# Optimization experiments

Measured on AMD Instinct MI355X. Metric: run time of the kernel, lower is better.

Reference implementation:

```python
import jax, jax.numpy as jnp
import numpy as np

B, N, GN, GS = 16, 100000, 4096, 64  # batch, points, num_groups, group_size


def setup_inputs() -> dict:
    key = jax.random.key(0)
    k1, k2, k3 = jax.random.split(key, 3)
    x_proto = jax.random.normal(k1, (B, N, 3), dtype=jnp.float32)
    template = jax.random.normal(k2, (N, 3), dtype=jnp.float32)
    groups = jax.random.randint(k3, (GN, GS), 0, N, dtype=jnp.int32)
    return {"x_proto": x_proto, "template": template, "groups": groups}


def reference(x_proto, template, groups):
    # x_proto: [B, N, 3], template: [N, 3], groups: [GN, GS] int indices
    b, n, _ = x_proto.shape
    Yg = template[groups]                      # [GN, GS, 3] gathered template
    Xg = x_proto[:, groups]                    # [B, GN, GS, 3] gathered current points

    # Kabsch: align template group Y to current X (R @ Y + t ~ X)
    muY = Yg.mean(axis=1)                      # [GN, 3]
    muX = Xg.mean(axis=2)                      # [B, GN, 3]
    Yc = Yg - muY[:, None, :]
    Xc = Xg - muX[:, :, None, :]
    H = jnp.einsum('gni,bgnj->bgij', Yc, Xc)   # [B, GN, 3, 3] covariance
    U, S, Vh = jnp.linalg.svd(H)
    V = jnp.swapaxes(Vh, -2, -1)
    R0 = V @ jnp.swapaxes(U, -2, -1)
    det = jnp.linalg.det(R0)                   # [B, GN]
    # flip last column of V where det < 0 to get a proper rotation
    s = jnp.where(det < 0, -1.0, 1.0).astype(x_proto.dtype)
    col_scale = jnp.stack([jnp.ones_like(s), jnp.ones_like(s), s], axis=-1)  # [B, GN, 3]
    R = (V * col_scale[..., None, :]) @ jnp.swapaxes(U, -2, -1)              # [B, GN, 3, 3]
    t = muX - jnp.einsum('bgij,gj->bgi', R, muY)                             # [B, GN, 3]

    # project template group through (R, t)
    Xg_proj = jnp.einsum('bgij,gnj->bgni', R, Yg) + t[:, :, None, :]         # [B, GN, GS, 3]

    # scatter-add with overlap counting, then average
    flat_idx = groups.reshape(-1)              # [GN*GS]
    out = jnp.zeros_like(x_proto).at[:, flat_idx].add(Xg_proj.reshape(b, -1, 3))
    counts = jnp.zeros((n,), dtype=x_proto.dtype).at[flat_idx].add(1.0)
    counts = jnp.maximum(counts, 1.0)
    return out / counts[None, :, None]
```

## Files before the change

kernel.cpp:

```cpp
#include <hip/hip_runtime.h>
#include <math.h>

static constexpr int BB = 16;
static constexpr int NN = 100000;
static constexpr int GN = 4096;
static constexpr int GS = 64;
static constexpr int NP = BB * GN;
static constexpr int NE = GN * GS;
static constexpr int NBLK = (NN + 255) / 256;

__device__ __forceinline__ float wsum64(float v) {
#pragma unroll
  for (int off = 32; off > 0; off >>= 1) v += __shfl_xor(v, off, 64);
  return v;
}

__global__ __launch_bounds__(256) void k_xpad(
    const float4* __restrict__ x, const float4* __restrict__ tpl,
    float4* __restrict__ x4, float4* __restrict__ tpl4,
    int4* __restrict__ cnt4, int* __restrict__ gtotal) {
  int t = blockIdx.x * 256 + threadIdx.x;
  if (t == 0) *gtotal = 0;
  if (t < NN / 4) {
    cnt4[t] = make_int4(0, 0, 0, 0);
    float4 a = tpl[t * 3 + 0], b = tpl[t * 3 + 1], c = tpl[t * 3 + 2];
    tpl4[t * 4 + 0] = make_float4(a.x, a.y, a.z, 0.f);
    tpl4[t * 4 + 1] = make_float4(a.w, b.x, b.y, 0.f);
    tpl4[t * 4 + 2] = make_float4(b.z, b.w, c.x, 0.f);
    tpl4[t * 4 + 3] = make_float4(c.y, c.z, c.w, 0.f);
  }
  if (t >= BB * NN / 4) return;
  float4 a = x[t * 3 + 0], b = x[t * 3 + 1], c = x[t * 3 + 2];
  x4[t * 4 + 0] = make_float4(a.x, a.y, a.z, 0.f);
  x4[t * 4 + 1] = make_float4(a.w, b.x, b.y, 0.f);
  x4[t * 4 + 2] = make_float4(b.z, b.w, c.x, 0.f);
  x4[t * 4 + 3] = make_float4(c.y, c.z, c.w, 0.f);
}

__global__ __launch_bounds__(256) void k_tpl(
    const float4* __restrict__ tpl4, const int* __restrict__ groups,
    float* __restrict__ Yg, float* __restrict__ GmY, int* __restrict__ cnt) {
  int g    = blockIdx.x * 4 + (threadIdx.x >> 6);
  int lane = threadIdx.x & 63;
  int idx = groups[g * GS + lane];
  atomicAdd(&cnt[idx], 1);
  float4 y = tpl4[idx];
  float* o = Yg + ((size_t)g * GS + lane) * 3;
  o[0] = y.x; o[1] = y.y; o[2] = y.z;
  float sy0 = wsum64(y.x), sy1 = wsum64(y.y), sy2 = wsum64(y.z);
  if (lane == 0) {
    const float inv = 1.0f / 64.0f;
    *(float4*)(GmY + (size_t)g * 4) =
        make_float4(sy0 * inv, sy1 * inv, sy2 * inv, 0.0f);
  }
}

__global__ __launch_bounds__(256) void k_stats(
    const float4* __restrict__ x4, const float* __restrict__ Yg,
    const float* __restrict__ GmY, const int* __restrict__ groups,
    float* __restrict__ Ht) {
  int bid  = (blockIdx.x & 7) * 512 + (blockIdx.x >> 3);
  int wid4 = bid * 4 + (threadIdx.x >> 6);
  int lane = threadIdx.x & 63;
  int s    = lane >> 4;
  int l4   = lane & 15;
  int p = wid4 * 4 + s;
  int b = p >> 12;
  int g = p & (GN - 1);

  int4 iv = *(const int4*)(groups + (size_t)g * GS + l4 * 4);
  const float4* yv = (const float4*)(Yg + ((size_t)g * GS + l4 * 4) * 3);
  float4 ya = yv[0], yb = yv[1], yc = yv[2];

  const float4* xb4 = x4 + (size_t)b * NN;
  float sx0 = 0.f, sx1 = 0.f, sx2 = 0.f;
  float h00 = 0.f, h01 = 0.f, h02 = 0.f;
  float h10 = 0.f, h11 = 0.f, h12 = 0.f;
  float h20 = 0.f, h21 = 0.f, h22 = 0.f;

#define ACC(Y0, Y1, Y2, IDX)                                   \
  {                                                            \
    float4 xv = xb4[IDX];                                      \
    sx0 += xv.x; sx1 += xv.y; sx2 += xv.z;                     \
    h00 += (Y0) * xv.x; h01 += (Y0) * xv.y; h02 += (Y0) * xv.z;\
    h10 += (Y1) * xv.x; h11 += (Y1) * xv.y; h12 += (Y1) * xv.z;\
    h20 += (Y2) * xv.x; h21 += (Y2) * xv.y; h22 += (Y2) * xv.z;\
  }
  ACC(ya.x, ya.y, ya.z, iv.x);
  ACC(ya.w, yb.x, yb.y, iv.y);
  ACC(yb.z, yb.w, yc.x, iv.z);
  ACC(yc.y, yc.z, yc.w, iv.w);
#undef ACC

#define RED(V)                                                 \
  V += __shfl_xor(V, 8, 64); V += __shfl_xor(V, 4, 64);        \
  V += __shfl_xor(V, 2, 64); V += __shfl_xor(V, 1, 64);
  RED(sx0) RED(sx1) RED(sx2)
  RED(h00) RED(h01) RED(h02)
  RED(h10) RED(h11) RED(h12)
  RED(h20) RED(h21) RED(h22)
#undef RED

  if (l4 == 0) {
    const float inv = 1.0f / 64.0f;
    float4 m = *(const float4*)(GmY + (size_t)g * 4);
    float mx0 = sx0 * inv, mx1 = sx1 * inv, mx2 = sx2 * inv;
    float4 o0 = make_float4(mx0, mx1, mx2, h00 - m.x * sx0);
    float4 o1 = make_float4(h01 - m.x * sx1, h02 - m.x * sx2,
                            h10 - m.y * sx0, h11 - m.y * sx1);
    float4 o2 = make_float4(h12 - m.y * sx2, h20 - m.z * sx0,
                            h21 - m.z * sx1, h22 - m.z * sx2);
    float* o = Ht + (size_t)p * 12;
    *(float4*)(o + 0) = o0;
    *(float4*)(o + 4) = o1;
    *(float4*)(o + 8) = o2;
  }
}

#define JROT(P, Q, RR)                                                        \
  {                                                                           \
    float apq = K[P][Q];                                                      \
    if (fabsf(apq) > 1e-30f) {                                                \
      float app = K[P][P], aqq = K[Q][Q];                                     \
      float tau = (aqq - app) / (2.0f * apq);                                 \
      float tt = copysignf(1.0f, tau) / (fabsf(tau) + sqrtf(1.0f + tau*tau)); \
      float cc = 1.0f / sqrtf(1.0f + tt * tt);                                \
      float ss = tt * cc;                                                     \
      K[P][P] = app - tt * apq;                                               \
      K[Q][Q] = aqq + tt * apq;                                               \
      K[P][Q] = 0.0f; K[Q][P] = 0.0f;                                         \
      float krp = K[RR][P], krq = K[RR][Q];                                   \
      K[RR][P] = cc * krp - ss * krq; K[P][RR] = K[RR][P];                    \
      K[RR][Q] = ss * krp + cc * krq; K[Q][RR] = K[RR][Q];                    \
      float v0p = V[0][P], v0q = V[0][Q];                                     \
      float v1p = V[1][P], v1q = V[1][Q];                                     \
      float v2p = V[2][P], v2q = V[2][Q];                                     \
      V[0][P] = cc * v0p - ss * v0q; V[0][Q] = ss * v0p + cc * v0q;           \
      V[1][P] = cc * v1p - ss * v1q; V[1][Q] = ss * v1p + cc * v1q;           \
      V[2][P] = cc * v2p - ss * v2q; V[2][Q] = ss * v2p + cc * v2q;           \
    }                                                                         \
  }

#define FIN(AA, BBi, CC)                                                      \
  {                                                                           \
    float va0 = V[0][AA], va1 = V[1][AA], va2 = V[2][AA];                     \
    float vb0 = V[0][BBi], vb1 = V[1][BBi], vb2 = V[2][BBi];                  \
    float vc0 = V[0][CC], vc1 = V[1][CC], vc2 = V[2][CC];                     \
    float ua0 = A[0][0]*va0 + A[0][1]*va1 + A[0][2]*va2;                      \
    float ua1 = A[1][0]*va0 + A[1][1]*va1 + A[1][2]*va2;                      \
    float ua2 = A[2][0]*va0 + A[2][1]*va1 + A[2][2]*va2;                      \
    float il = 1.0f / sqrtf(ua0*ua0 + ua1*ua1 + ua2*ua2 + 1e-30f);            \
    ua0 *= il; ua1 *= il; ua2 *= il;                                          \
    float ub0 = A[0][0]*vb0 + A[0][1]*vb1 + A[0][2]*vb2;                      \
    float ub1 = A[1][0]*vb0 + A[1][1]*vb1 + A[1][2]*vb2;                      \
    float ub2 = A[2][0]*vb0 + A[2][1]*vb1 + A[2][2]*vb2;                      \
    il = 1.0f / sqrtf(ub0*ub0 + ub1*ub1 + ub2*ub2 + 1e-30f);                  \
    ub0 *= il; ub1 *= il; ub2 *= il;                                          \
    float dd = ua0*ub0 + ua1*ub1 + ua2*ub2;                                   \
    ub0 -= dd * ua0; ub1 -= dd * ua1; ub2 -= dd * ua2;                        \
    il = 1.0f / sqrtf(ub0*ub0 + ub1*ub1 + ub2*ub2 + 1e-30f);                  \
    ub0 *= il; ub1 *= il; ub2 *= il;                                          \
    float uc0 = ua1*ub2 - ua2*ub1;                                            \
    float uc1 = ua2*ub0 - ua0*ub2;                                            \
    float uc2 = ua0*ub1 - ua1*ub0;                                            \
    R[0][0] = va0*ua0 + vb0*ub0 + dsg*vc0*uc0;                                \
    R[0][1] = va0*ua1 + vb0*ub1 + dsg*vc0*uc1;                                \
    R[0][2] = va0*ua2 + vb0*ub2 + dsg*vc0*uc2;                                \
    R[1][0] = va1*ua0 + vb1*ub0 + dsg*vc1*uc0;                                \
    R[1][1] = va1*ua1 + vb1*ub1 + dsg*vc1*uc1;                                \
    R[1][2] = va1*ua2 + vb1*ub2 + dsg*vc1*uc2;                                \
    R[2][0] = va2*ua0 + vb2*ub0 + dsg*vc2*uc0;                                \
    R[2][1] = va2*ua1 + vb2*ub1 + dsg*vc2*uc1;                                \
    R[2][2] = va2*ua2 + vb2*ub2 + dsg*vc2*uc2;                                \
  }

__global__ __launch_bounds__(256) void k_svd(
    const float* __restrict__ Ht, const float* __restrict__ GmY,
    float* __restrict__ Qt) {
  int p = blockIdx.x * 256 + threadIdx.x;
  if (p >= NP) return;
  int g = p & (GN - 1);
  const float* h = Ht + (size_t)p * 12;
  float4 f0 = *(const float4*)(h + 0);
  float4 f1 = *(const float4*)(h + 4);
  float4 f2 = *(const float4*)(h + 8);
  float4 m  = *(const float4*)(GmY + (size_t)g * 4);
  float mx0 = f0.x, mx1 = f0.y, mx2 = f0.z;
  float my0 = m.x, my1 = m.y, my2 = m.z;
  float A[3][3];
  A[0][0] = f0.w; A[0][1] = f1.x; A[0][2] = f1.y;
  A[1][0] = f1.z; A[1][1] = f1.w; A[1][2] = f2.x;
  A[2][0] = f2.y; A[2][1] = f2.z; A[2][2] = f2.w;

  float K[3][3];
#pragma unroll
  for (int i = 0; i < 3; ++i)
#pragma unroll
    for (int j = 0; j < 3; ++j)
      K[i][j] = A[0][i]*A[0][j] + A[1][i]*A[1][j] + A[2][i]*A[2][j];

  float V[3][3] = {{1.f,0.f,0.f},{0.f,1.f,0.f},{0.f,0.f,1.f}};
#pragma unroll
  for (int sweep = 0; sweep < 5; ++sweep) {
    JROT(0, 1, 2);
    JROT(0, 2, 1);
    JROT(1, 2, 0);
  }

  float d0 = K[0][0], d1 = K[1][1], d2 = K[2][2];
  float detV = V[0][0]*(V[1][1]*V[2][2] - V[1][2]*V[2][1])
             - V[0][1]*(V[1][0]*V[2][2] - V[1][2]*V[2][0])
             + V[0][2]*(V[1][0]*V[2][1] - V[1][1]*V[2][0]);
  float dsg = (detV < 0.0f) ? -1.0f : 1.0f;

  float R[3][3];
  if (d0 <= d1 && d0 <= d2) {
    FIN(1, 2, 0);
  } else if (d1 <= d0 && d1 <= d2) {
    FIN(2, 0, 1);
  } else {
    FIN(0, 1, 2);
  }

  float t0 = mx0 - (R[0][0]*my0 + R[0][1]*my1 + R[0][2]*my2);
  float t1 = mx1 - (R[1][0]*my0 + R[1][1]*my1 + R[1][2]*my2);
  float t2 = mx2 - (R[2][0]*my0 + R[2][1]*my1 + R[2][2]*my2);

  float qw, qx, qy, qz;
  float tr = R[0][0] + R[1][1] + R[2][2];
  if (tr > 0.f) {
    float S = sqrtf(tr + 1.0f) * 2.0f;
    qw = 0.25f * S;
    qx = (R[2][1] - R[1][2]) / S;
    qy = (R[0][2] - R[2][0]) / S;
    qz = (R[1][0] - R[0][1]) / S;
  } else if (R[0][0] > R[1][1] && R[0][0] > R[2][2]) {
    float S = sqrtf(1.0f + R[0][0] - R[1][1] - R[2][2]) * 2.0f;
    qw = (R[2][1] - R[1][2]) / S;
    qx = 0.25f * S;
    qy = (R[0][1] + R[1][0]) / S;
    qz = (R[0][2] + R[2][0]) / S;
  } else if (R[1][1] > R[2][2]) {
    float S = sqrtf(1.0f + R[1][1] - R[0][0] - R[2][2]) * 2.0f;
    qw = (R[0][2] - R[2][0]) / S;
    qx = (R[0][1] + R[1][0]) / S;
    qy = 0.25f * S;
    qz = (R[1][2] + R[2][1]) / S;
  } else {
    float S = sqrtf(1.0f + R[2][2] - R[0][0] - R[1][1]) * 2.0f;
    qw = (R[1][0] - R[0][1]) / S;
    qx = (R[0][2] + R[2][0]) / S;
    qy = (R[1][2] + R[2][1]) / S;
    qz = 0.25f * S;
  }
  float il2 = 1.0f / sqrtf(qw*qw + qx*qx + qy*qy + qz*qz);
  qw *= il2; qx *= il2; qy *= il2; qz *= il2;

  float* o = Qt + (size_t)p * 8;
  *(float4*)(o + 0) = make_float4(qx, qy, qz, qw);
  *(float4*)(o + 4) = make_float4(t0, t1, t2, 0.f);
}

__global__ __launch_bounds__(256) void k_alloc(
    const int* __restrict__ cnt, int* __restrict__ gtotal,
    int2* __restrict__ rs_cnt, int* __restrict__ cursor,
    int* __restrict__ entries) {
  int t = blockIdx.x * 256 + threadIdx.x;
  int lane = threadIdx.x & 63;
  int v  = (t < NN) ? cnt[t] : 0;
  int vp = (v + 3) & ~3;
  int sc = vp;
#pragma unroll
  for (int off = 1; off < 64; off <<= 1) {
    int u = __shfl_up(sc, off, 64);
    if (lane >= off) sc += u;
  }
  int wtotal = __shfl(sc, 63, 64);
  int base = 0;
  if (lane == 63) base = atomicAdd(gtotal, wtotal);
  base = __shfl(base, 63, 64);
  if (t < NN) {
    int s = base + sc - vp;
    rs_cnt[t] = make_int2(s, v);
    cursor[t] = 0;
    for (int k = v; k < vp; ++k) entries[s + k] = 0;
  }
}

__global__ __launch_bounds__(256) void k_fill(
    const int* __restrict__ groups, const int2* __restrict__ rs_cnt,
    int* __restrict__ cursor, int* __restrict__ entries) {
  int e = blockIdx.x * 256 + threadIdx.x;
  if (e >= NE) return;
  int n = groups[e];
  int pos = atomicAdd(&cursor[n], 1);
  entries[rs_cnt[n].x + pos] = e >> 6;
}

__global__ __launch_bounds__(256) void k_gather(
    const float4* __restrict__ tpl4, const int2* __restrict__ rs_cnt,
    const int* __restrict__ entries, const float* __restrict__ Qt,
    float* __restrict__ out) {
  int n = blockIdx.x * 256 + threadIdx.x;
  if (n >= NN) return;
  int b = blockIdx.y;
  int2 rc = rs_cnt[n];
  int s = rc.x, c = rc.y;
  float4 y = tpl4[n];
  float p0 = 0.f, p1 = 0.f, p2 = 0.f;
  const float* Qb = Qt + (size_t)b * GN * 8;

  for (int j = 0; j < c; j += 4) {
    int4 ev = *(const int4*)(entries + s + j);
    const float* qp0 = Qb + (size_t)ev.x * 8;
    const float* qp1 = Qb + (size_t)ev.y * 8;
    const float* qp2 = Qb + (size_t)ev.z * 8;
    const float* qp3 = Qb + (size_t)ev.w * 8;
    float4 qa = *(const float4*)(qp0);
    float4 ta = *(const float4*)(qp0 + 4);
    float4 qb = *(const float4*)(qp1);
    float4 tb = *(const float4*)(qp1 + 4);
    float4 qc = *(const float4*)(qp2);
    float4 tc = *(const float4*)(qp2 + 4);
    float4 qd = *(const float4*)(qp3);
    float4 td = *(const float4*)(qp3 + 4);
#define QACC(Q, T, K)                                                   \
    {                                                                   \
      float w = (j + (K) < c) ? 1.f : 0.f;                              \
      float tx = 2.f * ((Q).y * y.z - (Q).z * y.y);                     \
      float ty = 2.f * ((Q).z * y.x - (Q).x * y.z);                     \
      float tz = 2.f * ((Q).x * y.y - (Q).y * y.x);                     \
      p0 += w * (y.x + (Q).w * tx + ((Q).y * tz - (Q).z * ty) + (T).x); \
      p1 += w * (y.y + (Q).w * ty + ((Q).z * tx - (Q).x * tz) + (T).y); \
      p2 += w * (y.z + (Q).w * tz + ((Q).x * ty - (Q).y * tx) + (T).z); \
    }
    QACC(qa, ta, 0)
    QACC(qb, tb, 1)
    QACC(qc, tc, 2)
    QACC(qd, td, 3)
#undef QACC
  }
  float inv = 1.0f / fmaxf((float)c, 1.0f);
  float* o = out + ((size_t)b * NN + (size_t)n) * 3;
  *(float3*)o = make_float3(p0 * inv, p1 * inv, p2 * inv);
}

extern "C" void kernel_launch(void* const* d_in, const int* in_sizes, int n_in,
                              void* d_out, int out_size, void* d_ws, size_t ws_size,
                              hipStream_t stream) {
  const float* x      = (const float*)d_in[0];
  const float* tpl    = (const float*)d_in[1];
  const int*   groups = (const int*)d_in[2];
  float* out = (float*)d_out;

  char* ws = (char*)d_ws;
  size_t o_x4   = 0;
  size_t o_tpl4 = o_x4 + 25600000;
  size_t o_yg   = o_tpl4 + 1600000;
  size_t o_ht   = o_yg + 3145728;
  size_t o_qt   = o_ht + 3145728;
  size_t o_gmy  = o_qt + 2097152;
  size_t o_cnt  = o_gmy + 65536;
  size_t o_rsc  = o_cnt + 400000;
  size_t o_cur  = o_rsc + 800000;
  size_t o_gt   = o_cur + 400000;
  size_t o_ent  = o_gt + 64;
  float* x4     = (float*)(ws + o_x4);
  float* tpl4   = (float*)(ws + o_tpl4);
  float* Yg     = (float*)(ws + o_yg);
  float* Ht     = (float*)(ws + o_ht);
  float* Qt     = (float*)(ws + o_qt);
  float* GmY    = (float*)(ws + o_gmy);
  int*   cnt    = (int*)(ws + o_cnt);
  int2*  rs_cnt = (int2*)(ws + o_rsc);
  int*   cursor = (int*)(ws + o_cur);
  int*   gtotal = (int*)(ws + o_gt);
  int*   entries= (int*)(ws + o_ent);

  k_xpad<<<(BB * NN / 4 + 255) / 256, 256, 0, stream>>>(
      (const float4*)x, (const float4*)tpl, (float4*)x4, (float4*)tpl4,
      (int4*)cnt, gtotal);
  k_tpl<<<GN / 4, 256, 0, stream>>>((const float4*)tpl4, groups, Yg, GmY, cnt);
  k_stats<<<NP / 16, 256, 0, stream>>>((const float4*)x4, Yg, GmY, groups, Ht);
  k_alloc<<<NBLK, 256, 0, stream>>>(cnt, gtotal, rs_cnt, cursor, entries);
  k_fill<<<NE / 256, 256, 0, stream>>>(groups, rs_cnt, cursor, entries);
  k_svd<<<NP / 256, 256, 0, stream>>>(Ht, GmY, Qt);
  k_gather<<<dim3(NBLK, BB), 256, 0, stream>>>(
      (const float4*)tpl4, rs_cnt, entries, Qt, out);
}
```

Baseline: 141.5 us.

## Drop padded x/template copies, record atomic slot positions, XCD-aware gather order

Removes the k_xpad pass that rewrote the full x array (about 19 MB read, 25 MB written) and the template into float4-padded buffers. k_stats and k_gather now read the original 3-float layout directly with float3 loads. The return value of the counting atomic in k_tpl is stored per entry, so k_fill no longer needs a second atomic pass over a cursor array, and the cursor zeroing goes away. The gather grid is remapped so each XCD handles two batches, improving L2 locality for Qt. The cost is unaligned, uncoalesced 12-byte gathers in place of aligned 16-byte loads.

```diff
diff --git a/kernel.cpp b/kernel.cpp
--- a/kernel.cpp
+++ b/kernel.cpp
@@ -15,36 +15,24 @@
   return v;
 }
 
-__global__ __launch_bounds__(256) void k_xpad(
-    const float4* __restrict__ x, const float4* __restrict__ tpl,
-    float4* __restrict__ x4, float4* __restrict__ tpl4,
+__global__ __launch_bounds__(256) void k_zero(
     int4* __restrict__ cnt4, int* __restrict__ gtotal) {
   int t = blockIdx.x * 256 + threadIdx.x;
   if (t == 0) *gtotal = 0;
-  if (t < NN / 4) {
-    cnt4[t] = make_int4(0, 0, 0, 0);
-    float4 a = tpl[t * 3 + 0], b = tpl[t * 3 + 1], c = tpl[t * 3 + 2];
-    tpl4[t * 4 + 0] = make_float4(a.x, a.y, a.z, 0.f);
-    tpl4[t * 4 + 1] = make_float4(a.w, b.x, b.y, 0.f);
-    tpl4[t * 4 + 2] = make_float4(b.z, b.w, c.x, 0.f);
-    tpl4[t * 4 + 3] = make_float4(c.y, c.z, c.w, 0.f);
-  }
-  if (t >= BB * NN / 4) return;
-  float4 a = x[t * 3 + 0], b = x[t * 3 + 1], c = x[t * 3 + 2];
-  x4[t * 4 + 0] = make_float4(a.x, a.y, a.z, 0.f);
-  x4[t * 4 + 1] = make_float4(a.w, b.x, b.y, 0.f);
-  x4[t * 4 + 2] = make_float4(b.z, b.w, c.x, 0.f);
-  x4[t * 4 + 3] = make_float4(c.y, c.z, c.w, 0.f);
+  if (t < NN / 4) cnt4[t] = make_int4(0, 0, 0, 0);
 }
 
 __global__ __launch_bounds__(256) void k_tpl(
-    const float4* __restrict__ tpl4, const int* __restrict__ groups,
-    float* __restrict__ Yg, float* __restrict__ GmY, int* __restrict__ cnt) {
+    const float* __restrict__ tpl, const int* __restrict__ groups,
+    float* __restrict__ Yg, float* __restrict__ GmY,
+    int* __restrict__ cnt, int* __restrict__ epos) {
   int g    = blockIdx.x * 4 + (threadIdx.x >> 6);
   int lane = threadIdx.x & 63;
-  int idx = groups[g * GS + lane];
-  atomicAdd(&cnt[idx], 1);
-  float4 y = tpl4[idx];
+  int e    = g * GS + lane;
+  int idx = groups[e];
+  int pos = atomicAdd(&cnt[idx], 1);
+  epos[e] = pos;
+  float3 y = *(const float3*)(tpl + (size_t)idx * 3);
   float* o = Yg + ((size_t)g * GS + lane) * 3;
   o[0] = y.x; o[1] = y.y; o[2] = y.z;
   float sy0 = wsum64(y.x), sy1 = wsum64(y.y), sy2 = wsum64(y.z);
@@ -56,7 +44,7 @@
 }
 
 __global__ __launch_bounds__(256) void k_stats(
-    const float4* __restrict__ x4, const float* __restrict__ Yg,
+    const float* __restrict__ x, const float* __restrict__ Yg,
     const float* __restrict__ GmY, const int* __restrict__ groups,
     float* __restrict__ Ht) {
   int bid  = (blockIdx.x & 7) * 512 + (blockIdx.x >> 3);
@@ -72,7 +60,7 @@
   const float4* yv = (const float4*)(Yg + ((size_t)g * GS + l4 * 4) * 3);
   float4 ya = yv[0], yb = yv[1], yc = yv[2];
 
-  const float4* xb4 = x4 + (size_t)b * NN;
+  const float* xb = x + (size_t)b * NN * 3;
   float sx0 = 0.f, sx1 = 0.f, sx2 = 0.f;
   float h00 = 0.f, h01 = 0.f, h02 = 0.f;
   float h10 = 0.f, h11 = 0.f, h12 = 0.f;
@@ -80,7 +68,7 @@
 
 #define ACC(Y0, Y1, Y2, IDX)                                   \
   {                                                            \
-    float4 xv = xb4[IDX];                                      \
+    float3 xv = *(const float3*)(xb + (size_t)(IDX) * 3);      \
     sx0 += xv.x; sx1 += xv.y; sx2 += xv.z;                     \
     h00 += (Y0) * xv.x; h01 += (Y0) * xv.y; h02 += (Y0) * xv.z;\
     h10 += (Y1) * xv.x; h11 += (Y1) * xv.y; h12 += (Y1) * xv.z;\
@@ -263,8 +251,7 @@
 
 __global__ __launch_bounds__(256) void k_alloc(
     const int* __restrict__ cnt, int* __restrict__ gtotal,
-    int2* __restrict__ rs_cnt, int* __restrict__ cursor,
-    int* __restrict__ entries) {
+    int2* __restrict__ rs_cnt, int* __restrict__ entries) {
   int t = blockIdx.x * 256 + threadIdx.x;
   int lane = threadIdx.x & 63;
   int v  = (t < NN) ? cnt[t] : 0;
@@ -282,31 +269,33 @@
   if (t < NN) {
     int s = base + sc - vp;
     rs_cnt[t] = make_int2(s, v);
-    cursor[t] = 0;
     for (int k = v; k < vp; ++k) entries[s + k] = 0;
   }
 }
 
 __global__ __launch_bounds__(256) void k_fill(
     const int* __restrict__ groups, const int2* __restrict__ rs_cnt,
-    int* __restrict__ cursor, int* __restrict__ entries) {
+    const int* __restrict__ epos, int* __restrict__ entries) {
   int e = blockIdx.x * 256 + threadIdx.x;
   if (e >= NE) return;
   int n = groups[e];
-  int pos = atomicAdd(&cursor[n], 1);
-  entries[rs_cnt[n].x + pos] = e >> 6;
+  entries[rs_cnt[n].x + epos[e]] = e >> 6;
 }
 
 __global__ __launch_bounds__(256) void k_gather(
-    const float4* __restrict__ tpl4, const int2* __restrict__ rs_cnt,
+    const float* __restrict__ tpl, const int2* __restrict__ rs_cnt,
     const int* __restrict__ entries, const float* __restrict__ Qt,
     float* __restrict__ out) {
-  int n = blockIdx.x * 256 + threadIdx.x;
+  int bid = blockIdx.x;
+  int xcd = bid & 7;
+  int i   = bid >> 3;
+  int b   = xcd * 2 + (i / NBLK);
+  int nb  = i % NBLK;
+  int n   = nb * 256 + threadIdx.x;
   if (n >= NN) return;
-  int b = blockIdx.y;
   int2 rc = rs_cnt[n];
   int s = rc.x, c = rc.y;
-  float4 y = tpl4[n];
+  float3 y = *(const float3*)(tpl + (size_t)n * 3);
   float p0 = 0.f, p1 = 0.f, p2 = 0.f;
   const float* Qb = Qt + (size_t)b * GN * 8;
 
@@ -354,37 +343,30 @@
   float* out = (float*)d_out;
 
   char* ws = (char*)d_ws;
-  size_t o_x4   = 0;
-  size_t o_tpl4 = o_x4 + 25600000;
-  size_t o_yg   = o_tpl4 + 1600000;
+  size_t o_yg   = 0;
   size_t o_ht   = o_yg + 3145728;
   size_t o_qt   = o_ht + 3145728;
   size_t o_gmy  = o_qt + 2097152;
   size_t o_cnt  = o_gmy + 65536;
   size_t o_rsc  = o_cnt + 400000;
-  size_t o_cur  = o_rsc + 800000;
-  size_t o_gt   = o_cur + 400000;
-  size_t o_ent  = o_gt + 64;
-  float* x4     = (float*)(ws + o_x4);
-  float* tpl4   = (float*)(ws + o_tpl4);
+  size_t o_gt   = o_rsc + 800000;
+  size_t o_epos = o_gt + 64;
+  size_t o_ent  = o_epos + 1048576;
   float* Yg     = (float*)(ws + o_yg);
   float* Ht     = (float*)(ws + o_ht);
   float* Qt     = (float*)(ws + o_qt);
   float* GmY    = (float*)(ws + o_gmy);
   int*   cnt    = (int*)(ws + o_cnt);
   int2*  rs_cnt = (int2*)(ws + o_rsc);
-  int*   cursor = (int*)(ws + o_cur);
   int*   gtotal = (int*)(ws + o_gt);
+  int*   epos   = (int*)(ws + o_epos);
   int*   entries= (int*)(ws + o_ent);
 
-  k_xpad<<<(BB * NN / 4 + 255) / 256, 256, 0, stream>>>(
-      (const float4*)x, (const float4*)tpl, (float4*)x4, (float4*)tpl4,
-      (int4*)cnt, gtotal);
-  k_tpl<<<GN / 4, 256, 0, stream>>>((const float4*)tpl4, groups, Yg, GmY, cnt);
-  k_stats<<<NP / 16, 256, 0, stream>>>((const float4*)x4, Yg, GmY, groups, Ht);
-  k_alloc<<<NBLK, 256, 0, stream>>>(cnt, gtotal, rs_cnt, cursor, entries);
-  k_fill<<<NE / 256, 256, 0, stream>>>(groups, rs_cnt, cursor, entries);
+  k_zero<<<(NN / 4 + 255) / 256, 256, 0, stream>>>((int4*)cnt, gtotal);
+  k_tpl<<<GN / 4, 256, 0, stream>>>(tpl, groups, Yg, GmY, cnt, epos);
+  k_stats<<<NP / 16, 256, 0, stream>>>(x, Yg, GmY, groups, Ht);
   k_svd<<<NP / 256, 256, 0, stream>>>(Ht, GmY, Qt);
-  k_gather<<<dim3(NBLK, BB), 256, 0, stream>>>(
-      (const float4*)tpl4, rs_cnt, entries, Qt, out);
-}
+  k_alloc<<<NBLK, 256, 0, stream>>>(cnt, gtotal, rs_cnt, entries);
+  k_fill<<<NE / 256, 256, 0, stream>>>(groups, rs_cnt, epos, entries);
+  k_gather<<<8 * 2 * NBLK, 256, 0, stream>>>(tpl, rs_cnt, entries, Qt, out);
+}
```

Measured after the change: 122.5 us. 13.4% less time.
